# Performance work log

Measured on AMD Instinct MI355X. Metric: run time of the kernel, lower is better.

Reference implementation:

```python
import jax, jax.numpy as jnp
import numpy as np

DIM = 1024
N_STATE = 64
B, T = 16, 2048


def setup_inputs() -> dict:
    key = jax.random.key(0)
    ks = jax.random.split(key, 8)
    def xavier(k, shape):
        fan_in, fan_out = shape[1], shape[0]
        limit = float(np.sqrt(6.0 / (fan_in + fan_out)))
        return jax.random.uniform(k, shape, jnp.float32, -limit, limit)
    return {
        "x": jax.random.normal(ks[0], (B, T, DIM), jnp.float32),
        "W_in": xavier(ks[1], (DIM, DIM)),          # in_proj weight [d_inner, dim]
        "W_k": xavier(ks[2], (N_STATE, DIM)),
        "W_v": xavier(ks[3], (N_STATE, DIM)),
        "W_q": xavier(ks[4], (N_STATE, DIM)),
        "W_alpha": xavier(ks[5], (N_STATE, DIM)),
        "d_alpha": jnp.full((N_STATE,), 0.1, jnp.float32),
        "b_alpha": jnp.full((N_STATE,), 2.0, jnp.float32),
        "W_out": xavier(ks[6], (DIM, N_STATE)),      # out_proj weight [dim, n_state]
    }


def reference(x, W_in, W_k, W_v, W_q, W_alpha, d_alpha, b_alpha, W_out):
    # in_proj + silu: [B,T,D] -> [B,T,d_inner]
    xp = jax.nn.silu(jnp.einsum('btd,ed->bte', x, W_in))
    # precompute all projections, time-major [T,B,n]
    k_all = jnp.einsum('bte,ne->tbn', xp, W_k)
    v_all = jnp.einsum('bte,ne->tbn', xp, W_v)
    q_all = jnp.einsum('bte,ne->tbn', xp, W_q)
    ax_all = jnp.einsum('bte,ne->tbn', xp, W_alpha)

    S0 = jnp.zeros((x.shape[0], N_STATE, N_STATE), xp.dtype)

    def step(S, inp):
        k, v, q, ax = inp
        retrieved = jnp.einsum('bij,bj->bi', S, k)
        alpha = jax.nn.sigmoid(ax + d_alpha * retrieved + b_alpha)  # [B,n]
        a = alpha[..., None]
        S = a * S + (1.0 - a) * (v[..., None] * k[:, None, :])  # gated outer-product update
        o = jnp.einsum('bij,bj->bi', S, q)
        o = o * jax.nn.silu(o)
        return S, o

    S_final, outs = jax.lax.scan(step, S0, (k_all, v_all, q_all, ax_all))
    cell_out = jnp.transpose(outs, (1, 0, 2))  # [B,T,n]
    output = jnp.einsum('btn,dn->btd', cell_out, W_out)
    return output, S_final
```

## Files before the change

kernel.cpp:

```cpp
#include <hip/hip_runtime.h>
#include <hip/hip_bf16.h>

typedef unsigned short u16;
typedef __bf16 bf16x8 __attribute__((ext_vector_type(8)));
typedef float f32x4 __attribute__((ext_vector_type(4)));

__device__ inline u16 f2b(float f) {
    __hip_bfloat16 h = __float2bfloat16(f);
    return *(u16*)&h;
}

#define BM 128
#define BN 128
#define BK 32
#define LDSS 40

template<int AF32, int EPI>
__global__ __launch_bounds__(256) void gemm_bt(const void* __restrict__ Av,
                                               const u16* __restrict__ W,
                                               void* __restrict__ Cv,
                                               int M, int N, int K) {
    __shared__ u16 lds_a[BM * LDSS];
    __shared__ u16 lds_b[BN * LDSS];
    const int tid  = threadIdx.x;
    const int wave = tid >> 6;
    const int lane = tid & 63;
    const int wr = wave >> 1, wc = wave & 1;
    const int quad = lane >> 4, l15 = lane & 15;
    const int bm = blockIdx.x * BM;
    const int bn = blockIdx.y * BN;

    f32x4 acc[4][4] = {};

    const int lrow = tid >> 2;
    const int lch  = tid & 3;

    for (int k0 = 0; k0 < K; k0 += BK) {
        __syncthreads();
        if (AF32) {
            const float* Af = (const float*)Av;
            const int srow = tid >> 3;
            const int sch  = tid & 7;
            #pragma unroll
            for (int p = 0; p < 4; ++p) {
                const int r = p * 32 + srow;
                float4 va = *(const float4*)&Af[(size_t)(bm + r) * K + k0 + sch * 4];
                ushort4 pk = make_ushort4(f2b(va.x), f2b(va.y), f2b(va.z), f2b(va.w));
                *(ushort4*)&lds_a[r * LDSS + sch * 4] = pk;
            }
        } else {
            const u16* Ab = (const u16*)Av;
            *(uint4*)&lds_a[lrow * LDSS + lch * 8] =
                *(const uint4*)&Ab[(size_t)(bm + lrow) * K + k0 + lch * 8];
            *(uint4*)&lds_a[(lrow + 64) * LDSS + lch * 8] =
                *(const uint4*)&Ab[(size_t)(bm + lrow + 64) * K + k0 + lch * 8];
        }
        *(uint4*)&lds_b[lrow * LDSS + lch * 8] =
            *(const uint4*)&W[(size_t)(bn + lrow) * K + k0 + lch * 8];
        *(uint4*)&lds_b[(lrow + 64) * LDSS + lch * 8] =
            *(const uint4*)&W[(size_t)(bn + lrow + 64) * K + k0 + lch * 8];
        __syncthreads();

        bf16x8 af[4], bf[4];
        #pragma unroll
        for (int i = 0; i < 4; i++)
            af[i] = *(const bf16x8*)&lds_a[(wr * 64 + i * 16 + l15) * LDSS + quad * 8];
        #pragma unroll
        for (int j = 0; j < 4; j++)
            bf[j] = *(const bf16x8*)&lds_b[(wc * 64 + j * 16 + l15) * LDSS + quad * 8];
        #pragma unroll
        for (int i = 0; i < 4; i++)
            #pragma unroll
            for (int j = 0; j < 4; j++)
                acc[i][j] = __builtin_amdgcn_mfma_f32_16x16x32_bf16(af[i], bf[j], acc[i][j], 0, 0, 0);
    }

    #pragma unroll
    for (int i = 0; i < 4; i++) {
        #pragma unroll
        for (int j = 0; j < 4; j++) {
            #pragma unroll
            for (int r = 0; r < 4; r++) {
                const int row = bm + wr * 64 + i * 16 + quad * 4 + r;
                const int col = bn + wc * 64 + j * 16 + l15;
                float v = acc[i][j][r];
                if (EPI == 1) {
                    v = v / (1.f + __expf(-v));
                    ((__hip_bfloat16*)Cv)[(size_t)row * N + col] = __float2bfloat16(v);
                } else {
                    ((float*)Cv)[(size_t)row * N + col] = v;
                }
            }
        }
    }
}

__global__ __launch_bounds__(256) void convert_w(const float* __restrict__ Win,
                                                 const float* __restrict__ Wk,
                                                 const float* __restrict__ Wv,
                                                 const float* __restrict__ Wq,
                                                 const float* __restrict__ Wa,
                                                 const float* __restrict__ Wout,
                                                 u16* __restrict__ Win16,
                                                 u16* __restrict__ Wc16,
                                                 u16* __restrict__ Wout16) {
    int idx = blockIdx.x * 256 + threadIdx.x;
    if (idx < 1048576) { Win16[idx] = f2b(Win[idx]); return; }
    int i2 = idx - 1048576;
    if (i2 < 262144) {
        int which = i2 >> 16;
        int off = i2 & 65535;
        const float* s = (which == 0) ? Wk : (which == 1) ? Wv : (which == 2) ? Wq : Wa;
        Wc16[i2] = f2b(s[off]);
        return;
    }
    int i3 = i2 - 262144;
    Wout16[i3] = f2b(Wout[i3]);
}

#define T_LEN 2048
#define NS 64
#define PF 8

template<int CTRL>
__device__ inline float dpp_add(float x) {
    return x + __int_as_float(__builtin_amdgcn_mov_dpp(__float_as_int(x), CTRL, 0xf, 0xf, true));
}
__device__ inline float reduce8(float x) {
    x = dpp_add<0xB1>(x);
    x = dpp_add<0x4E>(x);
    x = dpp_add<0x128>(x);
    return x;
}

__global__ __launch_bounds__(64, 1) void scan_kernel(const float* __restrict__ P,
                                                     const float* __restrict__ d_alpha,
                                                     const float* __restrict__ b_alpha,
                                                     __hip_bfloat16* __restrict__ cell,
                                                     float* __restrict__ Sout) {
    const int blk = blockIdx.x;
    const int b = blk & 15;
    const int w = blk >> 4;
    const int lane = threadIdx.x;
    const int c = (lane & 3) | ((lane >> 1) & 4);
    const int r = ((lane >> 2) & 1) | ((lane >> 3) & 6);
    const int i = w * 8 + r;
    const int kc = c * 8;

    const float da = d_alpha[i];
    const float ba = b_alpha[i];
    const float* Pb = P + (size_t)b * T_LEN * 256;

    float s[8];
    #pragma unroll
    for (int j = 0; j < 8; j++) s[j] = 0.f;

    float4 ka[PF], kb[PF], qa[PF], qb[PF];
    float  vv[PF], aa[PF];

#define PREFETCH(p, tn) do {                                   \
        const float* row_ = &Pb[(size_t)(tn) * 256];           \
        ka[p] = *(const float4*)&row_[kc];                     \
        kb[p] = *(const float4*)&row_[kc + 4];                 \
        qa[p] = *(const float4*)&row_[128 + kc];               \
        qb[p] = *(const float4*)&row_[128 + kc + 4];           \
        vv[p] = row_[64 + i];                                  \
        aa[p] = row_[192 + i];                                 \
    } while (0)

#define SCAN_STEP(p, t, PRE) do {                              \
        const float4 k0 = ka[p], k1 = kb[p];                   \
        const float4 q0 = qa[p], q1 = qb[p];                   \
        const float v = vv[p], ax = aa[p];                     \
        PRE;                                                   \
        float rpa = s[0]*k0.x + s[1]*k0.y + s[2]*k0.z + s[3]*k0.w; \
        float rpb = s[4]*k1.x + s[5]*k1.y + s[6]*k1.z + s[7]*k1.w; \
        float rp = reduce8(rpa + rpb);                         \
        const float alpha = 1.f / (1.f + __expf(-(ax + da * rp + ba))); \
        const float cvk = (1.f - alpha) * v;                   \
        s[0] = alpha * s[0] + cvk * k0.x;                      \
        s[1] = alpha * s[1] + cvk * k0.y;                      \
        s[2] = alpha * s[2] + cvk * k0.z;                      \
        s[3] = alpha * s[3] + cvk * k0.w;                      \
        s[4] = alpha * s[4] + cvk * k1.x;                      \
        s[5] = alpha * s[5] + cvk * k1.y;                      \
        s[6] = alpha * s[6] + cvk * k1.z;                      \
        s[7] = alpha * s[7] + cvk * k1.w;                      \
        float opa = s[0]*q0.x + s[1]*q0.y + s[2]*q0.z + s[3]*q0.w; \
        float opb = s[4]*q1.x + s[5]*q1.y + s[6]*q1.z + s[7]*q1.w; \
        float op = reduce8(opa + opb);                         \
        const float sig = 1.f / (1.f + __expf(-op));           \
        const float o = op * op * sig;                         \
        if (c == 0)                                            \
            cell[(size_t)(b * T_LEN + (t)) * NS + i] = __float2bfloat16(o); \
    } while (0)

    #pragma unroll
    for (int p = 0; p < PF; ++p) PREFETCH(p, p);

    for (int t0 = 0; t0 < T_LEN - PF; t0 += PF) {
        #pragma unroll
        for (int p = 0; p < PF; ++p) {
            const int t = t0 + p;
            SCAN_STEP(p, t, PREFETCH(p, t + PF));
        }
    }
    #pragma unroll
    for (int p = 0; p < PF; ++p) {
        const int t = T_LEN - PF + p;
        SCAN_STEP(p, t, (void)0);
    }

#undef SCAN_STEP
#undef PREFETCH

    float4 s0 = make_float4(s[0], s[1], s[2], s[3]);
    float4 s1 = make_float4(s[4], s[5], s[6], s[7]);
    *(float4*)&Sout[(size_t)b * 4096 + i * 64 + kc]     = s0;
    *(float4*)&Sout[(size_t)b * 4096 + i * 64 + kc + 4] = s1;
}

extern "C" void kernel_launch(void* const* d_in, const int* in_sizes, int n_in,
                              void* d_out, int out_size, void* d_ws, size_t ws_size,
                              hipStream_t stream) {
    const float* x     = (const float*)d_in[0];
    const float* W_in  = (const float*)d_in[1];
    const float* W_k   = (const float*)d_in[2];
    const float* W_v   = (const float*)d_in[3];
    const float* W_q   = (const float*)d_in[4];
    const float* W_a   = (const float*)d_in[5];
    const float* d_alpha = (const float*)d_in[6];
    const float* b_alpha = (const float*)d_in[7];
    const float* W_out = (const float*)d_in[8];

    char* ws = (char*)d_ws;
    u16*   xp     = (u16*)ws;
    float* P      = (float*)(ws + (size_t)67108864);
    u16*   Win16  = (u16*)(ws + (size_t)100663296);
    u16*   Wc16   = (u16*)(ws + (size_t)102760448);
    u16*   Wout16 = (u16*)(ws + (size_t)103284736);
    __hip_bfloat16* cell = (__hip_bfloat16*)ws;

    float* out  = (float*)d_out;
    float* Sout = out + (size_t)32768 * 1024;

    convert_w<<<dim3(5376), dim3(256), 0, stream>>>(W_in, W_k, W_v, W_q, W_a, W_out,
                                                    Win16, Wc16, Wout16);
    gemm_bt<1, 1><<<dim3(256, 8), dim3(256), 0, stream>>>((const void*)x, Win16, (void*)xp,
                                                          32768, 1024, 1024);
    gemm_bt<0, 0><<<dim3(256, 2), dim3(256), 0, stream>>>((const void*)xp, Wc16, (void*)P,
                                                          32768, 256, 1024);
    scan_kernel<<<dim3(128), dim3(64), 0, stream>>>(P, d_alpha, b_alpha, cell, Sout);
    gemm_bt<0, 0><<<dim3(256, 8), dim3(256), 0, stream>>>((const void*)cell, Wout16, (void*)out,
                                                          32768, 1024, 64);
}
```

Baseline: 916.8 us.

## Stream scan inputs through an LDS ring buffer via async global-to-LDS loads

```diff
diff --git a/kernel.cpp b/kernel.cpp
--- a/kernel.cpp
+++ b/kernel.cpp
@@ -120,7 +120,8 @@
 
 #define T_LEN 2048
 #define NS 64
-#define PF 8
+#define PFD 16
+#define SLOTS 32
 
 template<int CTRL>
 __device__ inline float dpp_add(float x) {
@@ -133,11 +134,13 @@
     return x;
 }
 
-__global__ __launch_bounds__(64, 1) void scan_kernel(const float* __restrict__ P,
-                                                     const float* __restrict__ d_alpha,
-                                                     const float* __restrict__ b_alpha,
-                                                     __hip_bfloat16* __restrict__ cell,
-                                                     float* __restrict__ Sout) {
+__global__ __launch_bounds__(64) void scan_kernel(const float* __restrict__ P,
+                                                  const float* __restrict__ d_alpha,
+                                                  const float* __restrict__ b_alpha,
+                                                  __hip_bfloat16* __restrict__ cell,
+                                                  float* __restrict__ Sout) {
+    __shared__ float ldsbuf[SLOTS * 256];
+
     const int blk = blockIdx.x;
     const int b = blk & 15;
     const int w = blk >> 4;
@@ -155,64 +158,75 @@
     #pragma unroll
     for (int j = 0; j < 8; j++) s[j] = 0.f;
 
-    float4 ka[PF], kb[PF], qa[PF], qb[PF];
-    float  vv[PF], aa[PF];
-
-#define PREFETCH(p, tn) do {                                   \
-        const float* row_ = &Pb[(size_t)(tn) * 256];           \
-        ka[p] = *(const float4*)&row_[kc];                     \
-        kb[p] = *(const float4*)&row_[kc + 4];                 \
-        qa[p] = *(const float4*)&row_[128 + kc];               \
-        qb[p] = *(const float4*)&row_[128 + kc + 4];           \
-        vv[p] = row_[64 + i];                                  \
-        aa[p] = row_[192 + i];                                 \
+    float4 kaA, kbA, qaA, qbA; float vvA, aaA;
+    float4 kaB, kbB, qaB, qbB; float vvB, aaB;
+
+#define DMA(tn) __builtin_amdgcn_global_load_lds( \
+        (const __attribute__((address_space(1))) void*)(Pb + (size_t)(tn) * 256 + lane * 4), \
+        (__attribute__((address_space(3))) void*)(&ldsbuf[((tn) & (SLOTS - 1)) * 256]), \
+        16, 0, 0)
+
+#define READ(tn, X) do {                                        \
+        const float* rp_ = &ldsbuf[((tn) & (SLOTS - 1)) * 256]; \
+        ka##X = *(const float4*)&rp_[kc];                       \
+        kb##X = *(const float4*)&rp_[kc + 4];                   \
+        qa##X = *(const float4*)&rp_[128 + kc];                 \
+        qb##X = *(const float4*)&rp_[128 + kc + 4];             \
+        vv##X = rp_[64 + i];                                    \
+        aa##X = rp_[192 + i];                                   \
     } while (0)
 
-#define SCAN_STEP(p, t, PRE) do {                              \
-        const float4 k0 = ka[p], k1 = kb[p];                   \
-        const float4 q0 = qa[p], q1 = qb[p];                   \
-        const float v = vv[p], ax = aa[p];                     \
-        PRE;                                                   \
-        float rpa = s[0]*k0.x + s[1]*k0.y + s[2]*k0.z + s[3]*k0.w; \
-        float rpb = s[4]*k1.x + s[5]*k1.y + s[6]*k1.z + s[7]*k1.w; \
-        float rp = reduce8(rpa + rpb);                         \
-        const float alpha = 1.f / (1.f + __expf(-(ax + da * rp + ba))); \
-        const float cvk = (1.f - alpha) * v;                   \
-        s[0] = alpha * s[0] + cvk * k0.x;                      \
-        s[1] = alpha * s[1] + cvk * k0.y;                      \
-        s[2] = alpha * s[2] + cvk * k0.z;                      \
-        s[3] = alpha * s[3] + cvk * k0.w;                      \
-        s[4] = alpha * s[4] + cvk * k1.x;                      \
-        s[5] = alpha * s[5] + cvk * k1.y;                      \
-        s[6] = alpha * s[6] + cvk * k1.z;                      \
-        s[7] = alpha * s[7] + cvk * k1.w;                      \
-        float opa = s[0]*q0.x + s[1]*q0.y + s[2]*q0.z + s[3]*q0.w; \
-        float opb = s[4]*q1.x + s[5]*q1.y + s[6]*q1.z + s[7]*q1.w; \
-        float op = reduce8(opa + opb);                         \
-        const float sig = 1.f / (1.f + __expf(-op));           \
-        const float o = op * op * sig;                         \
-        if (c == 0)                                            \
-            cell[(size_t)(b * T_LEN + (t)) * NS + i] = __float2bfloat16(o); \
+#define COMPUTE(t, X) do {                                                   \
+        float rpa_ = s[0]*ka##X.x + s[1]*ka##X.y + s[2]*ka##X.z + s[3]*ka##X.w; \
+        float rpb_ = s[4]*kb##X.x + s[5]*kb##X.y + s[6]*kb##X.z + s[7]*kb##X.w; \
+        float rp_ = reduce8(rpa_ + rpb_);                                    \
+        const float alpha_ = 1.f / (1.f + __expf(-(aa##X + da * rp_ + ba))); \
+        const float cvk_ = (1.f - alpha_) * vv##X;                           \
+        s[0] = alpha_ * s[0] + cvk_ * ka##X.x;                               \
+        s[1] = alpha_ * s[1] + cvk_ * ka##X.y;                               \
+        s[2] = alpha_ * s[2] + cvk_ * ka##X.z;                               \
+        s[3] = alpha_ * s[3] + cvk_ * ka##X.w;                               \
+        s[4] = alpha_ * s[4] + cvk_ * kb##X.x;                               \
+        s[5] = alpha_ * s[5] + cvk_ * kb##X.y;                               \
+        s[6] = alpha_ * s[6] + cvk_ * kb##X.z;                               \
+        s[7] = alpha_ * s[7] + cvk_ * kb##X.w;                               \
+        float opa_ = s[0]*qa##X.x + s[1]*qa##X.y + s[2]*qa##X.z + s[3]*qa##X.w; \
+        float opb_ = s[4]*qb##X.x + s[5]*qb##X.y + s[6]*qb##X.z + s[7]*qb##X.w; \
+        float op_ = reduce8(opa_ + opb_);                                    \
+        const float sig_ = 1.f / (1.f + __expf(-op_));                       \
+        const float o_ = op_ * op_ * sig_;                                   \
+        if (c == 0)                                                          \
+            cell[(size_t)(b * T_LEN + (t)) * NS + i] = __float2bfloat16(o_); \
     } while (0)
 
+#define STEP(t, C, N) do {                                \
+        DMA((t) + PFD);                                   \
+        asm volatile("s_waitcnt vmcnt(30)" ::: "memory"); \
+        READ((t) + 1, N);                                 \
+        COMPUTE(t, C);                                    \
+    } while (0)
+
     #pragma unroll
-    for (int p = 0; p < PF; ++p) PREFETCH(p, p);
-
-    for (int t0 = 0; t0 < T_LEN - PF; t0 += PF) {
-        #pragma unroll
-        for (int p = 0; p < PF; ++p) {
-            const int t = t0 + p;
-            SCAN_STEP(p, t, PREFETCH(p, t + PF));
-        }
-    }
-    #pragma unroll
-    for (int p = 0; p < PF; ++p) {
-        const int t = T_LEN - PF + p;
-        SCAN_STEP(p, t, (void)0);
-    }
-
-#undef SCAN_STEP
-#undef PREFETCH
+    for (int p = 0; p < PFD; ++p) DMA(p);
+    asm volatile("s_waitcnt vmcnt(0)" ::: "memory");
+    READ(0, A);
+
+    for (int t = 0; t < T_LEN - PFD; t += 2) {
+        STEP(t,     A, B);
+        STEP(t + 1, B, A);
+    }
+
+    asm volatile("s_waitcnt vmcnt(0)" ::: "memory");
+    for (int t = T_LEN - PFD; t < T_LEN - 1; ++t) {
+        COMPUTE(t, A);
+        READ(t + 1, A);
+    }
+    COMPUTE(T_LEN - 1, A);
+
+#undef STEP
+#undef COMPUTE
+#undef READ
+#undef DMA
 
     float4 s0 = make_float4(s[0], s[1], s[2], s[3]);
     float4 s1 = make_float4(s[4], s[5], s[6], s[7]);
```

New measurement: 1.162 ms. 1.27x slower.
